# Kernel tuning notes

Measured on AMD Instinct MI355X. Metric: run time of the kernel, lower is better.

Reference implementation:

```python
import jax, jax.numpy as jnp
import numpy as np

DIM = 1024
HEADS = 8
DIM_HEAD = 64
INNER = HEADS * DIM_HEAD  # 512


def setup_inputs() -> dict:
    key = jax.random.key(0)
    k1, k2, k3, k4 = jax.random.split(key, 4)
    x = jax.random.normal(k1, (4, 4096, DIM), dtype=jnp.float32)
    W_qkv = jax.random.normal(k2, (DIM, 3 * INNER), dtype=jnp.float32) * (DIM ** -0.5)
    W_out = jax.random.normal(k3, (INNER, DIM), dtype=jnp.float32) * (INNER ** -0.5)
    b_out = jax.random.normal(k4, (DIM,), dtype=jnp.float32) * 0.01
    return {"x": x, "W_qkv": W_qkv, "W_out": W_out, "b_out": b_out}


def reference(x, W_qkv, W_out, b_out):
    b, n, _ = x.shape
    qkv = x @ W_qkv                                   # [b, n, 3*inner]
    q, k, v = jnp.split(qkv, 3, axis=-1)              # each [b, n, inner]

    def to_heads(t):
        return t.reshape(b, n, HEADS, DIM_HEAD).transpose(0, 2, 1, 3)  # [b, h, n, d]

    q = jax.nn.elu(to_heads(q)) + 1.0
    k = jax.nn.elu(to_heads(k)) + 1.0
    v = to_heads(v)
    # kv summary matrix: [b, h, d, e]
    context = jnp.einsum('bhnd,bhne->bhde', k, v)
    out = jnp.einsum('bhde,bhnd->bhne', context, q)   # [b, h, n, e]
    out = out.transpose(0, 2, 1, 3).reshape(b, n, INNER)
    return out @ W_out + b_out
```

## Files before the change

### kernel.cpp

```cpp
#include <hip/hip_runtime.h>
#include <hip/hip_bf16.h>
#include <cstdint>

typedef __attribute__((ext_vector_type(4))) float f32x4;
typedef __attribute__((ext_vector_type(8))) short bf16x8;

__device__ __forceinline__ ushort f2bf(float f) {
  unsigned u = __builtin_bit_cast(unsigned, f);
  u += 0x7fffu + ((u >> 16) & 1u);
  return (ushort)(u >> 16);
}
__device__ __forceinline__ float bf2f(ushort h) {
  unsigned u = ((unsigned)h) << 16;
  return __builtin_bit_cast(float, u);
}

__device__ __forceinline__ void gload_lds16(const ushort* g, ushort* l) {
  __builtin_amdgcn_global_load_lds(
      (const __attribute__((address_space(1))) unsigned int*)g,
      (__attribute__((address_space(3))) unsigned int*)l, 16, 0, 0);
}

__device__ __forceinline__ void hard_barrier() {
  __builtin_amdgcn_sched_barrier(0);
  __builtin_amdgcn_s_barrier();
  __builtin_amdgcn_sched_barrier(0);
}

template <int N>
__device__ __forceinline__ void wait_vm() {
  if constexpr (N == 0) asm volatile("s_waitcnt vmcnt(0)" ::: "memory");
  else if constexpr (N == 6) asm volatile("s_waitcnt vmcnt(6)" ::: "memory");
  else static_assert(N < 0, "unsupported vmcnt");
}

__global__ __launch_bounds__(256) void cvt_x_kernel(const float4* __restrict__ x,
                                                    ushort4* __restrict__ xb, int n4) {
  int stride = gridDim.x * blockDim.x;
  for (int i = blockIdx.x * blockDim.x + threadIdx.x; i < n4; i += stride) {
    float4 f = x[i];
    ushort4 o;
    o.x = f2bf(f.x); o.y = f2bf(f.y); o.z = f2bf(f.z); o.w = f2bf(f.w);
    xb[i] = o;
  }
}

__global__ __launch_bounds__(256) void transpose_w_kernel(const float* __restrict__ W,
                                                          ushort* __restrict__ Wt) {
  __shared__ float tile[32][33];
  int n0 = blockIdx.x * 32;
  int k0 = blockIdx.y * 32;
  int tx = threadIdx.x;
  int ty = threadIdx.y;
  #pragma unroll
  for (int p = 0; p < 4; ++p) {
    int k = k0 + ty + p * 8;
    tile[ty + p * 8][tx] = W[(size_t)k * 1536 + n0 + tx];
  }
  __syncthreads();
  #pragma unroll
  for (int p = 0; p < 4; ++p) {
    int n = n0 + ty + p * 8;
    Wt[(size_t)n * 1024 + k0 + tx] = f2bf(tile[tx][ty + p * 8]);
  }
}

template <int LDA, int LDB, int NT>
__device__ __forceinline__ void gemm_core_m201(const ushort* __restrict__ A,
                                               const ushort* __restrict__ Bt,
                                               int row0, int col0, f32x4 acc[8][4],
                                               ushort* lds) {
  const int tid = threadIdx.x;
  const int l = tid & 63;
  const int wid = tid >> 6;
  const int fr = l & 15, fq = l >> 4;
  const int wr = wid >> 2, wc = wid & 3;

  const int srow = tid >> 2;
  const int lam = (tid & 3) ^ ((tid >> 3) & 3);
  const ushort* aG = A + (size_t)(row0 + srow) * LDA + lam * 8;
  const ushort* bG = Bt + (size_t)(col0 + srow) * LDB + lam * 8;

  auto stageA = [&](int tt, int kap) {
    ushort* d = lds + (tt & 1) * 32768 + kap * 8192 + tid * 8;
    const ushort* s = aG + tt * 64 + kap * 32;
    gload_lds16(s, d);
    gload_lds16(s + (size_t)128 * LDA, d + 4096);
  };
  auto stageB = [&](int tt, int kap) {
    ushort* d = lds + (tt & 1) * 32768 + 16384 + kap * 8192 + tid * 8;
    const ushort* s = bG + tt * 64 + kap * 32;
    gload_lds16(s, d);
    gload_lds16(s + (size_t)128 * LDB, d + 4096);
  };

  const int sig = fq ^ ((fr >> 1) & 3);
  const int aOff = wr * 4096 + fr * 32 + sig * 8;
  const int bOff = 16384 + wc * 2048 + fr * 32 + sig * 8;

  auto mfma16 = [&](const bf16x8 av[4], const bf16x8 bv[4], int mh) {
    __builtin_amdgcn_s_setprio(1);
    #pragma unroll
    for (int mm = 0; mm < 4; ++mm)
      #pragma unroll
      for (int n = 0; n < 4; ++n)
        acc[mh * 4 + mm][n] =
            __builtin_amdgcn_mfma_f32_16x16x32_bf16(av[mm], bv[n], acc[mh * 4 + mm][n], 0, 0, 0);
    __builtin_amdgcn_s_setprio(0);
  };

  stageB(0, 0); stageA(0, 0); stageB(0, 1); stageA(0, 1);
  stageB(1, 0); stageA(1, 0); stageB(1, 1);
  wait_vm<6>();
  hard_barrier();

  for (int t = 0; t < NT; ++t) {
    const ushort* sb = lds + (t & 1) * 32768;
    bf16x8 av[4], bv[4];

    #pragma unroll
    for (int mm = 0; mm < 4; ++mm) av[mm] = *(const bf16x8*)(sb + aOff + mm * 512);
    #pragma unroll
    for (int n = 0; n < 4; ++n) bv[n] = *(const bf16x8*)(sb + bOff + n * 512);
    if (t + 1 < NT) stageA(t + 1, 1);
    hard_barrier();
    mfma16(av, bv, 0);
    hard_barrier();

    #pragma unroll
    for (int mm = 0; mm < 4; ++mm) av[mm] = *(const bf16x8*)(sb + aOff + 2048 + mm * 512);
    if (t + 2 < NT) stageB(t + 2, 0);
    hard_barrier();
    mfma16(av, bv, 1);
    hard_barrier();

    #pragma unroll
    for (int mm = 0; mm < 4; ++mm) av[mm] = *(const bf16x8*)(sb + 8192 + aOff + mm * 512);
    #pragma unroll
    for (int n = 0; n < 4; ++n) bv[n] = *(const bf16x8*)(sb + 8192 + bOff + n * 512);
    if (t + 2 < NT) stageA(t + 2, 0);
    hard_barrier();
    mfma16(av, bv, 0);
    hard_barrier();

    #pragma unroll
    for (int mm = 0; mm < 4; ++mm) av[mm] = *(const bf16x8*)(sb + 8192 + aOff + 2048 + mm * 512);
    if (t + 2 < NT) { stageB(t + 2, 1); wait_vm<6>(); } else { wait_vm<0>(); }
    hard_barrier();
    mfma16(av, bv, 1);
    hard_barrier();
  }
}

__global__ __launch_bounds__(512, 1) void gemm_qkv_kernel(const ushort* __restrict__ xb,
                                                          const ushort* __restrict__ wt,
                                                          ushort* __restrict__ qkv) {
  __shared__ ushort lds[65536];
  f32x4 acc[8][4] = {};
  const int row0 = blockIdx.x * 256;
  const int col0 = blockIdx.y * 256;
  gemm_core_m201<1024, 1024, 16>(xb, wt, row0, col0, acc, lds);
  const int l = threadIdx.x & 63;
  const int wid = threadIdx.x >> 6;
  const int wr = wid >> 2, wc = wid & 3;
  const int fr = l & 15, fq = l >> 4;
  #pragma unroll
  for (int m = 0; m < 8; ++m) {
    #pragma unroll
    for (int n = 0; n < 4; ++n) {
      const int c = col0 + wc * 64 + n * 16 + fr;
      #pragma unroll
      for (int j = 0; j < 4; ++j) {
        const int r = row0 + wr * 128 + m * 16 + fq * 4 + j;
        float v = acc[m][n][j];
        if (c < 1024) v = (v > 0.f) ? (v + 1.f) : __expf(v);
        qkv[(size_t)r * 1536 + c] = f2bf(v);
      }
    }
  }
}

__global__ __launch_bounds__(256) void ctx_kernel(const ushort* __restrict__ qkv,
                                                  float* __restrict__ part) {
  const int bh = blockIdx.x;
  const int split = blockIdx.y;
  const int b = bh >> 3, h = bh & 7;
  const int t = threadIdx.x;
  const int d0 = (t >> 4) * 4;
  const int e0 = (t & 15) * 4;
  __shared__ ushort ks[64][64];
  __shared__ ushort vs[64][64];
  float acc[4][4] = {};
  const int rowBase = b * 4096 + split * 256;
  for (int chunk = 0; chunk < 256; chunk += 64) {
    __syncthreads();
    #pragma unroll
    for (int p = 0; p < 2; ++p) {
      const int r = (t >> 3) + p * 32;
      const int c = (t & 7) * 8;
      const ushort* src = qkv + (size_t)(rowBase + chunk + r) * 1536;
      *(uint4*)&ks[r][c] = *(const uint4*)(src + 512 + h * 64 + c);
      *(uint4*)&vs[r][c] = *(const uint4*)(src + 1024 + h * 64 + c);
    }
    __syncthreads();
    for (int r = 0; r < 64; ++r) {
      ushort4 ku = *(const ushort4*)&ks[r][d0];
      ushort4 vu = *(const ushort4*)&vs[r][e0];
      float kk[4] = {bf2f(ku.x), bf2f(ku.y), bf2f(ku.z), bf2f(ku.w)};
      float vv[4] = {bf2f(vu.x), bf2f(vu.y), bf2f(vu.z), bf2f(vu.w)};
      #pragma unroll
      for (int i = 0; i < 4; ++i)
        #pragma unroll
        for (int j = 0; j < 4; ++j)
          acc[i][j] += kk[i] * vv[j];
    }
  }
  float* dst = part + ((size_t)split * 32 + bh) * 4096;
  #pragma unroll
  for (int i = 0; i < 4; ++i)
    #pragma unroll
    for (int j = 0; j < 4; ++j)
      dst[(d0 + i) * 64 + (e0 + j)] = acc[i][j];
}

__global__ __launch_bounds__(256) void ctx_reduce_kernel(const float* __restrict__ part,
                                                         float* __restrict__ ctx) {
  const int i = blockIdx.x * 256 + threadIdx.x;
  float s = 0.f;
  #pragma unroll
  for (int sp = 0; sp < 16; ++sp) s += part[(size_t)sp * 131072 + i];
  ctx[i] = s;
}

__global__ __launch_bounds__(256) void weff_kernel(const float* __restrict__ ctx,
                                                   const float* __restrict__ Wout,
                                                   ushort* __restrict__ weff) {
  const int bh = blockIdx.x;
  const int h = bh & 7;
  const int m0 = blockIdx.y * 128;
  const int t = threadIdx.x;
  __shared__ float cs[64 * 64];
  __shared__ float ws[64][128];
  #pragma unroll
  for (int p = 0; p < 4; ++p) {
    const int idx = p * 1024 + t * 4;
    *(float4*)&cs[idx] = *(const float4*)&ctx[(size_t)bh * 4096 + idx];
  }
  #pragma unroll
  for (int p = 0; p < 8; ++p) {
    const int e = (t >> 5) + p * 8;
    const int c = (t & 31) * 4;
    *(float4*)&ws[e][c] = *(const float4*)&Wout[(size_t)(h * 64 + e) * 1024 + m0 + c];
  }
  __syncthreads();
  const int m = t & 127;
  const int dh = (t >> 7) * 32;
  float acc[32] = {};
  for (int e = 0; e < 64; ++e) {
    const float w = ws[e][m];
    #pragma unroll
    for (int i = 0; i < 32; ++i)
      acc[i] += cs[(dh + i) * 64 + e] * w;
  }
  ushort* dst = weff + ((size_t)(bh >> 3) * 1024 + m0 + m) * 512 + h * 64 + dh;
  #pragma unroll
  for (int i = 0; i < 32; ++i) dst[i] = f2bf(acc[i]);
}

__global__ __launch_bounds__(512, 1) void gemm_out_kernel(const ushort* __restrict__ qkv,
                                                          const ushort* __restrict__ weff,
                                                          const float* __restrict__ bout,
                                                          float* __restrict__ out) {
  __shared__ ushort lds[65536];
  f32x4 acc[8][4] = {};
  const int row0 = blockIdx.x * 256;
  const int col0 = blockIdx.y * 256;
  const int b = row0 >> 12;
  gemm_core_m201<1536, 512, 8>(qkv, weff + (size_t)b * 1024 * 512, row0, col0, acc, lds);
  const int l = threadIdx.x & 63;
  const int wid = threadIdx.x >> 6;
  const int wr = wid >> 2, wc = wid & 3;
  const int fr = l & 15, fq = l >> 4;
  #pragma unroll
  for (int m = 0; m < 8; ++m) {
    #pragma unroll
    for (int n = 0; n < 4; ++n) {
      const int c = col0 + wc * 64 + n * 16 + fr;
      const float bb = bout[c];
      #pragma unroll
      for (int j = 0; j < 4; ++j) {
        const int r = row0 + wr * 128 + m * 16 + fq * 4 + j;
        out[(size_t)r * 1024 + c] = acc[m][n][j] + bb;
      }
    }
  }
}

extern "C" void kernel_launch(void* const* d_in, const int* in_sizes, int n_in,
                              void* d_out, int out_size, void* d_ws, size_t ws_size,
                              hipStream_t stream) {
  const float* x    = (const float*)d_in[0];
  const float* Wqkv = (const float*)d_in[1];
  const float* Wout = (const float*)d_in[2];
  const float* bout = (const float*)d_in[3];
  float* out = (float*)d_out;
  char* ws = (char*)d_ws;

  ushort* xb   = (ushort*)(ws);
  ushort* wt   = (ushort*)(ws + 33554432);
  ushort* qkv  = (ushort*)(ws + 36700160);
  float*  part = (float* )(ws + 87031808);
  float*  ctx  = (float* )(ws + 95420416);
  ushort* weff = (ushort*)(ws + 95944704);

  cvt_x_kernel<<<2048, 256, 0, stream>>>((const float4*)x, (ushort4*)xb, 16384 * 1024 / 4);
  transpose_w_kernel<<<dim3(48, 32), dim3(32, 8), 0, stream>>>(Wqkv, wt);
  gemm_qkv_kernel<<<dim3(64, 6), 512, 0, stream>>>(xb, wt, qkv);
  ctx_kernel<<<dim3(32, 16), 256, 0, stream>>>(qkv, part);
  ctx_reduce_kernel<<<512, 256, 0, stream>>>(part, ctx);
  weff_kernel<<<dim3(32, 8), 256, 0, stream>>>(ctx, Wout, weff);
  gemm_out_kernel<<<dim3(64, 4), 512, 0, stream>>>(qkv, weff, bout, out);
}
```

Before: 152.7 us.

## Switch GEMM core to 4-stage LDS ring with K=32 slices

Restructures the shared GEMM mainloop. The old core used two 64-wide K buffers with split A/B staging; the new one uses a four-slot ring of 32-wide K tiles and prefetches three tiles ahead, with the vmcnt waits adjusted to match. The goal is deeper prefetch, so global-to-LDS latency is better hidden behind MFMA work. In exchange, each iteration does half the K work, so per-iteration barrier and loop overhead doubles relative to compute.

```diff
diff --git a/kernel.cpp b/kernel.cpp
--- a/kernel.cpp
+++ b/kernel.cpp
@@ -30,7 +30,8 @@
 template <int N>
 __device__ __forceinline__ void wait_vm() {
   if constexpr (N == 0) asm volatile("s_waitcnt vmcnt(0)" ::: "memory");
-  else if constexpr (N == 6) asm volatile("s_waitcnt vmcnt(6)" ::: "memory");
+  else if constexpr (N == 4) asm volatile("s_waitcnt vmcnt(4)" ::: "memory");
+  else if constexpr (N == 8) asm volatile("s_waitcnt vmcnt(8)" ::: "memory");
   else static_assert(N < 0, "unsupported vmcnt");
 }
 
@@ -66,10 +67,10 @@
 }
 
 template <int LDA, int LDB, int NT>
-__device__ __forceinline__ void gemm_core_m201(const ushort* __restrict__ A,
-                                               const ushort* __restrict__ Bt,
-                                               int row0, int col0, f32x4 acc[8][4],
-                                               ushort* lds) {
+__device__ __forceinline__ void gemm_core4(const ushort* __restrict__ A,
+                                           const ushort* __restrict__ Bt,
+                                           int row0, int col0, f32x4 acc[8][4],
+                                           ushort* lds) {
   const int tid = threadIdx.x;
   const int l = tid & 63;
   const int wid = tid >> 6;
@@ -81,22 +82,22 @@
   const ushort* aG = A + (size_t)(row0 + srow) * LDA + lam * 8;
   const ushort* bG = Bt + (size_t)(col0 + srow) * LDB + lam * 8;
 
-  auto stageA = [&](int tt, int kap) {
-    ushort* d = lds + (tt & 1) * 32768 + kap * 8192 + tid * 8;
-    const ushort* s = aG + tt * 64 + kap * 32;
+  auto stageA = [&](int tt) {
+    ushort* d = lds + (tt & 3) * 16384 + tid * 8;
+    const ushort* s = aG + tt * 32;
     gload_lds16(s, d);
     gload_lds16(s + (size_t)128 * LDA, d + 4096);
   };
-  auto stageB = [&](int tt, int kap) {
-    ushort* d = lds + (tt & 1) * 32768 + 16384 + kap * 8192 + tid * 8;
-    const ushort* s = bG + tt * 64 + kap * 32;
+  auto stageB = [&](int tt) {
+    ushort* d = lds + (tt & 3) * 16384 + 8192 + tid * 8;
+    const ushort* s = bG + tt * 32;
     gload_lds16(s, d);
     gload_lds16(s + (size_t)128 * LDB, d + 4096);
   };
 
   const int sig = fq ^ ((fr >> 1) & 3);
   const int aOff = wr * 4096 + fr * 32 + sig * 8;
-  const int bOff = 16384 + wc * 2048 + fr * 32 + sig * 8;
+  const int bOff = 8192 + wc * 2048 + fr * 32 + sig * 8;
 
   auto mfma16 = [&](const bf16x8 av[4], const bf16x8 bv[4], int mh) {
     __builtin_amdgcn_s_setprio(1);
@@ -109,43 +110,33 @@
     __builtin_amdgcn_s_setprio(0);
   };
 
-  stageB(0, 0); stageA(0, 0); stageB(0, 1); stageA(0, 1);
-  stageB(1, 0); stageA(1, 0); stageB(1, 1);
-  wait_vm<6>();
+  stageA(0); stageB(0); stageA(1); stageB(1); stageA(2); stageB(2);
+  wait_vm<8>();
   hard_barrier();
 
   for (int t = 0; t < NT; ++t) {
-    const ushort* sb = lds + (t & 1) * 32768;
+    const ushort* sb = lds + (t & 3) * 16384;
     bf16x8 av[4], bv[4];
 
     #pragma unroll
     for (int mm = 0; mm < 4; ++mm) av[mm] = *(const bf16x8*)(sb + aOff + mm * 512);
     #pragma unroll
     for (int n = 0; n < 4; ++n) bv[n] = *(const bf16x8*)(sb + bOff + n * 512);
-    if (t + 1 < NT) stageA(t + 1, 1);
+    if (t + 3 < NT) stageA(t + 3);
     hard_barrier();
     mfma16(av, bv, 0);
     hard_barrier();
 
     #pragma unroll
     for (int mm = 0; mm < 4; ++mm) av[mm] = *(const bf16x8*)(sb + aOff + 2048 + mm * 512);
-    if (t + 2 < NT) stageB(t + 2, 0);
-    hard_barrier();
-    mfma16(av, bv, 1);
-    hard_barrier();
-
-    #pragma unroll
-    for (int mm = 0; mm < 4; ++mm) av[mm] = *(const bf16x8*)(sb + 8192 + aOff + mm * 512);
-    #pragma unroll
-    for (int n = 0; n < 4; ++n) bv[n] = *(const bf16x8*)(sb + 8192 + bOff + n * 512);
-    if (t + 2 < NT) stageA(t + 2, 0);
-    hard_barrier();
-    mfma16(av, bv, 0);
-    hard_barrier();
-
-    #pragma unroll
-    for (int mm = 0; mm < 4; ++mm) av[mm] = *(const bf16x8*)(sb + 8192 + aOff + 2048 + mm * 512);
-    if (t + 2 < NT) { stageB(t + 2, 1); wait_vm<6>(); } else { wait_vm<0>(); }
+    if (t + 3 < NT) {
+      stageB(t + 3);
+      wait_vm<8>();
+    } else if (t + 3 == NT) {
+      wait_vm<4>();
+    } else if (t + 2 == NT) {
+      wait_vm<0>();
+    }
     hard_barrier();
     mfma16(av, bv, 1);
     hard_barrier();
@@ -159,7 +150,7 @@
   f32x4 acc[8][4] = {};
   const int row0 = blockIdx.x * 256;
   const int col0 = blockIdx.y * 256;
-  gemm_core_m201<1024, 1024, 16>(xb, wt, row0, col0, acc, lds);
+  gemm_core4<1024, 1024, 32>(xb, wt, row0, col0, acc, lds);
   const int l = threadIdx.x & 63;
   const int wid = threadIdx.x >> 6;
   const int wr = wid >> 2, wc = wid & 3;
@@ -276,7 +267,7 @@
   const int row0 = blockIdx.x * 256;
   const int col0 = blockIdx.y * 256;
   const int b = row0 >> 12;
-  gemm_core_m201<1536, 512, 8>(qkv, weff + (size_t)b * 1024 * 512, row0, col0, acc, lds);
+  gemm_core4<1536, 512, 16>(qkv, weff + (size_t)b * 1024 * 512, row0, col0, acc, lds);
   const int l = threadIdx.x & 63;
   const int wid = threadIdx.x >> 6;
   const int wr = wid >> 2, wc = wid & 3;
```

After: 159.4 us. 1.04x slower.
